# Performance work log

Hardware: AMD Instinct MI355X
Metric: run time of the kernel (lower is better)

## Reference

```python
import jax, jax.numpy as jnp
import numpy as np


def setup_inputs() -> dict:
    key = jax.random.key(0)
    k1, k2, k3, k4 = jax.random.split(key, 4)
    B, S, D = 4, 2048, 1024
    return {
        "x": jax.random.normal(k1, (B, S, D), dtype=jnp.float32),
        "wq": jax.random.normal(k2, (D, D), dtype=jnp.float32),
        "wk": jax.random.normal(k3, (D, D), dtype=jnp.float32),
        "wv": jax.random.normal(k4, (D, D), dtype=jnp.float32),
    }


def reference(x, wq, wk, wv):
    # q,k,v: [B,S,D]
    q = x @ wq
    k = x @ wk
    v = x @ wv
    # NOTE: source applies NO 1/sqrt(d) scaling; we match it faithfully.
    scores = jnp.einsum("bsd,btd->bst", q, k)  # [B,S,S]
    weights = jax.nn.softmax(scores, axis=-1)
    return jnp.einsum("bst,btd->bsd", weights, v)  # [B,S,D]
```

## Files before the change

kernel.cpp:

```cpp
#include <hip/hip_runtime.h>


typedef _Float16 half4_t __attribute__((ext_vector_type(4)));
typedef _Float16 half8_t __attribute__((ext_vector_type(8)));
typedef float f32x4 __attribute__((ext_vector_type(4)));

#define BM 128
#define BN 128
#define BK 32

__device__ __forceinline__ void gl_lds16(const _Float16* g, _Float16* l) {
    __builtin_amdgcn_global_load_lds(
        (const __attribute__((address_space(1))) unsigned int*)g,
        (__attribute__((address_space(3))) unsigned int*)l, 16, 0, 0);
}


__global__ __launch_bounds__(256) void conv_split_kernel(
    const float* __restrict__ in, _Float16* __restrict__ hi,
    _Float16* __restrict__ lo, int n4)
{
    int i = blockIdx.x * 256 + threadIdx.x;
    if (i >= n4) return;
    float4 v = ((const float4*)in)[i];
    float xs[4] = {v.x, v.y, v.z, v.w};
    half4_t h, l;
#pragma unroll
    for (int j = 0; j < 4; ++j) {
        _Float16 hh = (_Float16)xs[j];
        h[j] = hh;
        l[j] = (_Float16)(xs[j] - (float)hh);
    }
    ((half4_t*)hi)[i] = h;
    ((half4_t*)lo)[i] = l;
}

__global__ __launch_bounds__(256) void conv_wvT_kernel(
    const float* __restrict__ w, _Float16* __restrict__ oh)
{
    __shared__ float tle[64][65];
    const int tr = blockIdx.y * 64, tc = blockIdx.x * 64;
    const int t16 = threadIdx.x & 15, tq = threadIdx.x >> 4;
#pragma unroll
    for (int j = 0; j < 4; ++j) {
        int lr = tq + j * 16;
        float4 v = *(const float4*)(w + (size_t)(tr + lr) * 1024 + tc + t16 * 4);
        tle[lr][t16 * 4 + 0] = v.x;
        tle[lr][t16 * 4 + 1] = v.y;
        tle[lr][t16 * 4 + 2] = v.z;
        tle[lr][t16 * 4 + 3] = v.w;
    }
    __syncthreads();
#pragma unroll
    for (int j = 0; j < 4; ++j) {
        int orow = tq + j * 16;
        int oc = t16 * 4;
        half4_t h;
#pragma unroll
        for (int i = 0; i < 4; ++i) h[i] = (_Float16)tle[oc + i][orow];
        *(half4_t*)(oh + (size_t)(tc + orow) * 1024 + tr + oc) = h;
    }
}

template <bool OUTF32>
__global__ __launch_bounds__(256) void gemm_split(
    const _Float16* __restrict__ Ah, const _Float16* __restrict__ Al, size_t az,
    const _Float16* __restrict__ Bh, const _Float16* __restrict__ Bl, size_t bz,
    float* __restrict__ Cf, size_t cz, int ldc,
    _Float16* __restrict__ Oh, _Float16* __restrict__ Ol, size_t oz, int ldo,
    int lda, int ldb, int K)
{
    __shared__ __align__(16) _Float16 sAh[BM][BK], sAl[BM][BK];
    __shared__ __align__(16) _Float16 sBh[BN][BK], sBl[BN][BK];

    const int tid = threadIdx.x;
    const int wave = tid >> 6, lane = tid & 63;
    const int wm = (wave >> 1) * 64, wn = (wave & 1) * 64;
    const int lrow = lane & 15, quad = lane >> 4;
    const int bm = blockIdx.y * BM, bn = blockIdx.x * BN;
    const int z = blockIdx.z;

    const _Float16* pAh = Ah + (size_t)z * az;
    const _Float16* pAl = Al + (size_t)z * az;
    const _Float16* pBh = Bh + (size_t)z * bz;
    const _Float16* pBl = Bl + (size_t)z * bz;

    const int r0 = wave * 32 + (lane >> 2);
    const int kofs = (lane & 3) * 8;
    const size_t a0o = (size_t)(bm + r0) * lda + kofs;
    const size_t a1o = a0o + (size_t)16 * lda;
    const size_t b0o = (size_t)(bn + r0) * ldb + kofs;
    const size_t b1o = b0o + (size_t)16 * ldb;
    _Float16* lA0 = &sAh[r0][kofs];
    _Float16* lA1 = &sAh[r0 + 16][kofs];
    _Float16* lAl0 = &sAl[r0][kofs];
    _Float16* lAl1 = &sAl[r0 + 16][kofs];
    _Float16* lB0 = &sBh[r0][kofs];
    _Float16* lB1 = &sBh[r0 + 16][kofs];
    _Float16* lBl0 = &sBl[r0][kofs];
    _Float16* lBl1 = &sBl[r0 + 16][kofs];

    f32x4 acc[4][4];
#pragma unroll
    for (int i = 0; i < 4; ++i)
#pragma unroll
        for (int j = 0; j < 4; ++j) acc[i][j] = 0.0f;

    for (int k0 = 0; k0 < K; k0 += BK) {
        gl_lds16(pAh + a0o + k0, lA0);
        gl_lds16(pAh + a1o + k0, lA1);
        gl_lds16(pAl + a0o + k0, lAl0);
        gl_lds16(pAl + a1o + k0, lAl1);
        gl_lds16(pBh + b0o + k0, lB0);
        gl_lds16(pBh + b1o + k0, lB1);
        gl_lds16(pBl + b0o + k0, lBl0);
        gl_lds16(pBl + b1o + k0, lBl1);
        __syncthreads();

        half8_t a0[4], a1[4], b0[4], b1[4];
#pragma unroll
        for (int mt = 0; mt < 4; ++mt) {
            a0[mt] = *(const half8_t*)&sAh[wm + mt * 16 + lrow][quad * 8];
            a1[mt] = *(const half8_t*)&sAl[wm + mt * 16 + lrow][quad * 8];
        }
#pragma unroll
        for (int nt = 0; nt < 4; ++nt) {
            b0[nt] = *(const half8_t*)&sBh[wn + nt * 16 + lrow][quad * 8];
            b1[nt] = *(const half8_t*)&sBl[wn + nt * 16 + lrow][quad * 8];
        }
#pragma unroll
        for (int mt = 0; mt < 4; ++mt)
#pragma unroll
            for (int nt = 0; nt < 4; ++nt) {
                acc[mt][nt] = __builtin_amdgcn_mfma_f32_16x16x32_f16(a0[mt], b0[nt], acc[mt][nt], 0, 0, 0);
                acc[mt][nt] = __builtin_amdgcn_mfma_f32_16x16x32_f16(a0[mt], b1[nt], acc[mt][nt], 0, 0, 0);
                acc[mt][nt] = __builtin_amdgcn_mfma_f32_16x16x32_f16(a1[mt], b0[nt], acc[mt][nt], 0, 0, 0);
            }
        __syncthreads();
    }

#pragma unroll
    for (int mt = 0; mt < 4; ++mt)
#pragma unroll
        for (int nt = 0; nt < 4; ++nt)
#pragma unroll
            for (int r = 0; r < 4; ++r) {
                int gm = bm + wm + mt * 16 + quad * 4 + r;
                int gn = bn + wn + nt * 16 + lrow;
                float v = acc[mt][nt][r];
                if (OUTF32) {
                    Cf[(size_t)z * cz + (size_t)gm * ldc + gn] = v;
                } else {
                    _Float16 h = (_Float16)v;
                    Oh[(size_t)z * oz + (size_t)gm * ldo + gn] = h;
                    Ol[(size_t)z * oz + (size_t)gm * ldo + gn] = (_Float16)(v - (float)h);
                }
            }
}

template <bool TRANSOUT>
__global__ __launch_bounds__(256) void gemm_plain(
    const _Float16* __restrict__ Ag, size_t az,
    const _Float16* __restrict__ Bg, size_t bz,
    float* __restrict__ Cf, size_t cz, int ldc,
    _Float16* __restrict__ Ot,
    int lda, int ldb, int K)
{
    __shared__ __align__(16) _Float16 sA[BM][BK], sB[BN][BK];

    const int tid = threadIdx.x;
    const int wave = tid >> 6, lane = tid & 63;
    const int wm = (wave >> 1) * 64, wn = (wave & 1) * 64;
    const int lrow = lane & 15, quad = lane >> 4;
    const int bm = blockIdx.y * BM, bn = blockIdx.x * BN;
    const int z = blockIdx.z;

    const _Float16* pA = Ag + (size_t)z * az;
    const _Float16* pB = Bg + (size_t)z * bz;

    const int r0 = wave * 32 + (lane >> 2);
    const int kofs = (lane & 3) * 8;
    const size_t a0o = (size_t)(bm + r0) * lda + kofs;
    const size_t a1o = a0o + (size_t)16 * lda;
    const size_t b0o = (size_t)(bn + r0) * ldb + kofs;
    const size_t b1o = b0o + (size_t)16 * ldb;
    _Float16* lA0 = &sA[r0][kofs];
    _Float16* lA1 = &sA[r0 + 16][kofs];
    _Float16* lB0 = &sB[r0][kofs];
    _Float16* lB1 = &sB[r0 + 16][kofs];

    f32x4 acc[4][4];
#pragma unroll
    for (int i = 0; i < 4; ++i)
#pragma unroll
        for (int j = 0; j < 4; ++j) acc[i][j] = 0.0f;

    for (int k0 = 0; k0 < K; k0 += BK) {
        gl_lds16(pA + a0o + k0, lA0);
        gl_lds16(pA + a1o + k0, lA1);
        gl_lds16(pB + b0o + k0, lB0);
        gl_lds16(pB + b1o + k0, lB1);
        __syncthreads();

        half8_t a0[4], b0[4];
#pragma unroll
        for (int mt = 0; mt < 4; ++mt)
            a0[mt] = *(const half8_t*)&sA[wm + mt * 16 + lrow][quad * 8];
#pragma unroll
        for (int nt = 0; nt < 4; ++nt)
            b0[nt] = *(const half8_t*)&sB[wn + nt * 16 + lrow][quad * 8];
#pragma unroll
        for (int mt = 0; mt < 4; ++mt)
#pragma unroll
            for (int nt = 0; nt < 4; ++nt)
                acc[mt][nt] = __builtin_amdgcn_mfma_f32_16x16x32_f16(a0[mt], b0[nt], acc[mt][nt], 0, 0, 0);
        __syncthreads();
    }

#pragma unroll
    for (int mt = 0; mt < 4; ++mt)
#pragma unroll
        for (int nt = 0; nt < 4; ++nt) {
            int gm0 = bm + wm + mt * 16 + quad * 4;
            int gn = bn + wn + nt * 16 + lrow;
            if (TRANSOUT) {
                half4_t o;
#pragma unroll
                for (int r = 0; r < 4; ++r) o[r] = (_Float16)acc[mt][nt][r];
                *(half4_t*)(Ot + ((size_t)(gm0 >> 11) << 21) +
                            (size_t)gn * 2048 + (gm0 & 2047)) = o;
            } else {
#pragma unroll
                for (int r = 0; r < 4; ++r)
                    Cf[(size_t)z * cz + (size_t)(gm0 + r) * ldc + gn] = acc[mt][nt][r];
            }
        }
}

__global__ __launch_bounds__(256) void softmax_kernel(float* __restrict__ S)
{
    float* row = S + (size_t)blockIdx.x * 2048;
    float4* r4 = (float4*)row;
    const int tid = threadIdx.x;
    const int wave = tid >> 6, lane = tid & 63;

    float4 a = r4[tid], b = r4[tid + 256];
    float m = fmaxf(fmaxf(fmaxf(a.x, a.y), fmaxf(a.z, a.w)),
                    fmaxf(fmaxf(b.x, b.y), fmaxf(b.z, b.w)));
#pragma unroll
    for (int o = 32; o; o >>= 1) m = fmaxf(m, __shfl_xor(m, o));
    __shared__ float redm[4];
    __shared__ float reds[4];
    if (lane == 0) redm[wave] = m;
    __syncthreads();
    m = fmaxf(fmaxf(redm[0], redm[1]), fmaxf(redm[2], redm[3]));

    a.x = __expf(a.x - m); a.y = __expf(a.y - m);
    a.z = __expf(a.z - m); a.w = __expf(a.w - m);
    b.x = __expf(b.x - m); b.y = __expf(b.y - m);
    b.z = __expf(b.z - m); b.w = __expf(b.w - m);

    float s = a.x + a.y + a.z + a.w + b.x + b.y + b.z + b.w;
#pragma unroll
    for (int o = 32; o; o >>= 1) s += __shfl_xor(s, o);
    if (lane == 0) reds[wave] = s;
    __syncthreads();
    s = reds[0] + reds[1] + reds[2] + reds[3];

    float inv = 1.0f / s;
    _Float16* o16 = (_Float16*)row;
    half4_t ha, hb;
    ha[0] = (_Float16)(a.x * inv); ha[1] = (_Float16)(a.y * inv);
    ha[2] = (_Float16)(a.z * inv); ha[3] = (_Float16)(a.w * inv);
    hb[0] = (_Float16)(b.x * inv); hb[1] = (_Float16)(b.y * inv);
    hb[2] = (_Float16)(b.z * inv); hb[3] = (_Float16)(b.w * inv);
    ((half4_t*)o16)[tid] = ha;
    ((half4_t*)o16)[tid + 256] = hb;
}

extern "C" void kernel_launch(void* const* d_in, const int* in_sizes, int n_in,
                              void* d_out, int out_size, void* d_ws, size_t ws_size,
                              hipStream_t stream)
{
    const float* x  = (const float*)d_in[0];
    const float* wq = (const float*)d_in[1];
    const float* wk = (const float*)d_in[2];
    const float* wv = (const float*)d_in[3];
    float* out = (float*)d_out;

    const int S = 2048, D = 1024;
    const size_t M8 = 8ull << 20;
    const size_t M1 = 1ull << 20;
    char* ws = (char*)d_ws;

    _Float16* xh   = (_Float16*)(ws);
    _Float16* xl   = (_Float16*)(ws + (16ull << 20));
    _Float16* yh   = (_Float16*)(ws + (32ull << 20));
    _Float16* yl   = (_Float16*)(ws + (48ull << 20));
    _Float16* vT   = (_Float16*)(ws + (64ull << 20));
    _Float16* wqh  = (_Float16*)(ws + (80ull << 20));
    _Float16* wql  = (_Float16*)(ws + (82ull << 20));
    _Float16* wkh  = (_Float16*)(ws + (84ull << 20));
    _Float16* wkl  = (_Float16*)(ws + (86ull << 20));
    _Float16* wvTh = (_Float16*)(ws + (88ull << 20));
    _Float16* Mh   = (_Float16*)(ws + (90ull << 20));
    _Float16* Ml   = (_Float16*)(ws + (92ull << 20));
    float*    sc   = (float*)(ws + (94ull << 20));

    dim3 blk(256);

    conv_split_kernel<<<dim3((int)(M8 / 4 / 256)), blk, 0, stream>>>(x, xh, xl, (int)(M8 / 4));
    conv_split_kernel<<<dim3((int)(M1 / 4 / 256)), blk, 0, stream>>>(wq, wqh, wql, (int)(M1 / 4));
    conv_split_kernel<<<dim3((int)(M1 / 4 / 256)), blk, 0, stream>>>(wk, wkh, wkl, (int)(M1 / 4));
    conv_wvT_kernel<<<dim3(16, 16), blk, 0, stream>>>(wv, wvTh);

    gemm_split<false><<<dim3(8, 8, 1), blk, 0, stream>>>(
        wkh, wkl, 0, wqh, wql, 0, nullptr, 0, 0, Mh, Ml, 0, D, D, D, D);

    gemm_split<false><<<dim3(D / BN, 8192 / BM, 1), blk, 0, stream>>>(
        xh, xl, 0, Mh, Ml, 0, nullptr, 0, 0, yh, yl, 0, D, D, D, D);

    gemm_plain<true><<<dim3(D / BN, 8192 / BM, 1), blk, 0, stream>>>(
        xh, 0, wvTh, 0, nullptr, 0, 0, vT, D, D, D);

    gemm_split<true><<<dim3(S / BN, S / BM, 4), blk, 0, stream>>>(
        yh, yl, (size_t)S * D, xh, xl, (size_t)S * D, sc, (size_t)S * S, S,
        nullptr, nullptr, 0, 0, D, D, D);

    softmax_kernel<<<dim3(4 * S), blk, 0, stream>>>(sc);

    gemm_plain<false><<<dim3(D / BN, S / BM, 4), blk, 0, stream>>>(
        (const _Float16*)sc, (size_t)S * 4096, vT, (size_t)D * S,
        out, (size_t)S * D, D, nullptr, 4096, S, S);
}
```

Measured before the change: 431.9 us.

## Widen GEMM tiles to 128x256 with 8 waves and fuse conversion kernels

Doubles the GEMM block N-tile to 256 and runs 512 threads (8 waves in a 2x4 grid), with the global-to-LDS load mapping rewritten for the larger tile. Each wave still computes a 64x64 subtile, but every A tile loaded into LDS is now reused across twice as many columns. The four fp32-to-fp16 conversion and transpose launches are merged into one role-dispatched kernel to cut launch count. In exchange LDS per block doubles, fewer blocks fit on a CU, and the small weight GEMM launches fewer blocks.

```diff
diff --git a/kernel.cpp b/kernel.cpp
--- a/kernel.cpp
+++ b/kernel.cpp
@@ -6,7 +6,7 @@
 typedef float f32x4 __attribute__((ext_vector_type(4)));
 
 #define BM 128
-#define BN 128
+#define BN 256
 #define BK 32
 
 __device__ __forceinline__ void gl_lds16(const _Float16* g, _Float16* l) {
@@ -15,55 +15,62 @@
         (__attribute__((address_space(3))) unsigned int*)l, 16, 0, 0);
 }
 
-
-__global__ __launch_bounds__(256) void conv_split_kernel(
-    const float* __restrict__ in, _Float16* __restrict__ hi,
-    _Float16* __restrict__ lo, int n4)
-{
-    int i = blockIdx.x * 256 + threadIdx.x;
-    if (i >= n4) return;
-    float4 v = ((const float4*)in)[i];
-    float xs[4] = {v.x, v.y, v.z, v.w};
-    half4_t h, l;
-#pragma unroll
-    for (int j = 0; j < 4; ++j) {
-        _Float16 hh = (_Float16)xs[j];
-        h[j] = hh;
-        l[j] = (_Float16)(xs[j] - (float)hh);
+__global__ __launch_bounds__(256) void conv_all_kernel(
+    const float* __restrict__ x, const float* __restrict__ wq,
+    const float* __restrict__ wk, const float* __restrict__ wv,
+    _Float16* __restrict__ xh, _Float16* __restrict__ xl,
+    _Float16* __restrict__ qh, _Float16* __restrict__ ql,
+    _Float16* __restrict__ kh, _Float16* __restrict__ kl,
+    _Float16* __restrict__ vTh)
+{
+    __shared__ float tle[64][65];
+    const int role = blockIdx.y;
+    if (role < 3) {
+        const float* in = (role == 0) ? x : (role == 1) ? wq : wk;
+        _Float16* hi = (role == 0) ? xh : (role == 1) ? qh : kh;
+        _Float16* lo = (role == 0) ? xl : (role == 1) ? ql : kl;
+        const int n4 = (role == 0) ? (1 << 21) : (1 << 18);
+        int i = blockIdx.x * 256 + threadIdx.x;
+        if (i >= n4) return;
+        float4 v = ((const float4*)in)[i];
+        float xs[4] = {v.x, v.y, v.z, v.w};
+        half4_t h, l;
+#pragma unroll
+        for (int j = 0; j < 4; ++j) {
+            _Float16 hh = (_Float16)xs[j];
+            h[j] = hh;
+            l[j] = (_Float16)(xs[j] - (float)hh);
+        }
+        ((half4_t*)hi)[i] = h;
+        ((half4_t*)lo)[i] = l;
+    } else {
+        if (blockIdx.x >= 256) return;
+        const int tr = (blockIdx.x >> 4) * 64, tc = (blockIdx.x & 15) * 64;
+        const int t16 = threadIdx.x & 15, tq = threadIdx.x >> 4;
+#pragma unroll
+        for (int j = 0; j < 4; ++j) {
+            int lr = tq + j * 16;
+            float4 v = *(const float4*)(wv + (size_t)(tr + lr) * 1024 + tc + t16 * 4);
+            tle[lr][t16 * 4 + 0] = v.x;
+            tle[lr][t16 * 4 + 1] = v.y;
+            tle[lr][t16 * 4 + 2] = v.z;
+            tle[lr][t16 * 4 + 3] = v.w;
+        }
+        __syncthreads();
+#pragma unroll
+        for (int j = 0; j < 4; ++j) {
+            int orow = tq + j * 16;
+            int oc = t16 * 4;
+            half4_t h;
+#pragma unroll
+            for (int i = 0; i < 4; ++i) h[i] = (_Float16)tle[oc + i][orow];
+            *(half4_t*)(vTh + (size_t)(tc + orow) * 1024 + tr + oc) = h;
+        }
     }
-    ((half4_t*)hi)[i] = h;
-    ((half4_t*)lo)[i] = l;
-}
-
-__global__ __launch_bounds__(256) void conv_wvT_kernel(
-    const float* __restrict__ w, _Float16* __restrict__ oh)
-{
-    __shared__ float tle[64][65];
-    const int tr = blockIdx.y * 64, tc = blockIdx.x * 64;
-    const int t16 = threadIdx.x & 15, tq = threadIdx.x >> 4;
-#pragma unroll
-    for (int j = 0; j < 4; ++j) {
-        int lr = tq + j * 16;
-        float4 v = *(const float4*)(w + (size_t)(tr + lr) * 1024 + tc + t16 * 4);
-        tle[lr][t16 * 4 + 0] = v.x;
-        tle[lr][t16 * 4 + 1] = v.y;
-        tle[lr][t16 * 4 + 2] = v.z;
-        tle[lr][t16 * 4 + 3] = v.w;
-    }
-    __syncthreads();
-#pragma unroll
-    for (int j = 0; j < 4; ++j) {
-        int orow = tq + j * 16;
-        int oc = t16 * 4;
-        half4_t h;
-#pragma unroll
-        for (int i = 0; i < 4; ++i) h[i] = (_Float16)tle[oc + i][orow];
-        *(half4_t*)(oh + (size_t)(tc + orow) * 1024 + tr + oc) = h;
-    }
 }
 
 template <bool OUTF32>
-__global__ __launch_bounds__(256) void gemm_split(
+__global__ __launch_bounds__(512, 5) void gemm_split(
     const _Float16* __restrict__ Ah, const _Float16* __restrict__ Al, size_t az,
     const _Float16* __restrict__ Bh, const _Float16* __restrict__ Bl, size_t bz,
     float* __restrict__ Cf, size_t cz, int ldc,
@@ -75,7 +82,7 @@
 
     const int tid = threadIdx.x;
     const int wave = tid >> 6, lane = tid & 63;
-    const int wm = (wave >> 1) * 64, wn = (wave & 1) * 64;
+    const int wm = (wave >> 2) * 64, wn = (wave & 3) * 64;
     const int lrow = lane & 15, quad = lane >> 4;
     const int bm = blockIdx.y * BM, bn = blockIdx.x * BN;
     const int z = blockIdx.z;
@@ -85,20 +92,17 @@
     const _Float16* pBh = Bh + (size_t)z * bz;
     const _Float16* pBl = Bl + (size_t)z * bz;
 
-    const int r0 = wave * 32 + (lane >> 2);
-    const int kofs = (lane & 3) * 8;
-    const size_t a0o = (size_t)(bm + r0) * lda + kofs;
-    const size_t a1o = a0o + (size_t)16 * lda;
-    const size_t b0o = (size_t)(bn + r0) * ldb + kofs;
-    const size_t b1o = b0o + (size_t)16 * ldb;
-    _Float16* lA0 = &sAh[r0][kofs];
-    _Float16* lA1 = &sAh[r0 + 16][kofs];
-    _Float16* lAl0 = &sAl[r0][kofs];
-    _Float16* lAl1 = &sAl[r0 + 16][kofs];
-    _Float16* lB0 = &sBh[r0][kofs];
-    _Float16* lB1 = &sBh[r0 + 16][kofs];
-    _Float16* lBl0 = &sBl[r0][kofs];
-    _Float16* lBl1 = &sBl[r0 + 16][kofs];
+    const int rowA = tid >> 2;
+    const int kofs = (tid & 3) * 8;
+    const size_t aoff  = (size_t)(bm + rowA) * lda + kofs;
+    const size_t boff0 = (size_t)(bn + rowA) * ldb + kofs;
+    const size_t boff1 = boff0 + (size_t)128 * ldb;
+    _Float16* lAh = &sAh[rowA][kofs];
+    _Float16* lAl = &sAl[rowA][kofs];
+    _Float16* lBh0 = &sBh[rowA][kofs];
+    _Float16* lBh1 = &sBh[rowA + 128][kofs];
+    _Float16* lBl0 = &sBl[rowA][kofs];
+    _Float16* lBl1 = &sBl[rowA + 128][kofs];
 
     f32x4 acc[4][4];
 #pragma unroll
@@ -107,14 +111,12 @@
         for (int j = 0; j < 4; ++j) acc[i][j] = 0.0f;
 
     for (int k0 = 0; k0 < K; k0 += BK) {
-        gl_lds16(pAh + a0o + k0, lA0);
-        gl_lds16(pAh + a1o + k0, lA1);
-        gl_lds16(pAl + a0o + k0, lAl0);
-        gl_lds16(pAl + a1o + k0, lAl1);
-        gl_lds16(pBh + b0o + k0, lB0);
-        gl_lds16(pBh + b1o + k0, lB1);
-        gl_lds16(pBl + b0o + k0, lBl0);
-        gl_lds16(pBl + b1o + k0, lBl1);
+        gl_lds16(pAh + aoff + k0, lAh);
+        gl_lds16(pAl + aoff + k0, lAl);
+        gl_lds16(pBh + boff0 + k0, lBh0);
+        gl_lds16(pBh + boff1 + k0, lBh1);
+        gl_lds16(pBl + boff0 + k0, lBl0);
+        gl_lds16(pBl + boff1 + k0, lBl1);
         __syncthreads();
 
         half8_t a0[4], a1[4], b0[4], b1[4];
@@ -159,7 +161,7 @@
 }
 
 template <bool TRANSOUT>
-__global__ __launch_bounds__(256) void gemm_plain(
+__global__ __launch_bounds__(512, 5) void gemm_plain(
     const _Float16* __restrict__ Ag, size_t az,
     const _Float16* __restrict__ Bg, size_t bz,
     float* __restrict__ Cf, size_t cz, int ldc,
@@ -170,7 +172,7 @@
 
     const int tid = threadIdx.x;
     const int wave = tid >> 6, lane = tid & 63;
-    const int wm = (wave >> 1) * 64, wn = (wave & 1) * 64;
+    const int wm = (wave >> 2) * 64, wn = (wave & 3) * 64;
     const int lrow = lane & 15, quad = lane >> 4;
     const int bm = blockIdx.y * BM, bn = blockIdx.x * BN;
     const int z = blockIdx.z;
@@ -178,16 +180,14 @@
     const _Float16* pA = Ag + (size_t)z * az;
     const _Float16* pB = Bg + (size_t)z * bz;
 
-    const int r0 = wave * 32 + (lane >> 2);
-    const int kofs = (lane & 3) * 8;
-    const size_t a0o = (size_t)(bm + r0) * lda + kofs;
-    const size_t a1o = a0o + (size_t)16 * lda;
-    const size_t b0o = (size_t)(bn + r0) * ldb + kofs;
-    const size_t b1o = b0o + (size_t)16 * ldb;
-    _Float16* lA0 = &sA[r0][kofs];
-    _Float16* lA1 = &sA[r0 + 16][kofs];
-    _Float16* lB0 = &sB[r0][kofs];
-    _Float16* lB1 = &sB[r0 + 16][kofs];
+    const int rowA = tid >> 2;
+    const int kofs = (tid & 3) * 8;
+    const size_t aoff  = (size_t)(bm + rowA) * lda + kofs;
+    const size_t boff0 = (size_t)(bn + rowA) * ldb + kofs;
+    const size_t boff1 = boff0 + (size_t)128 * ldb;
+    _Float16* lA  = &sA[rowA][kofs];
+    _Float16* lB0 = &sB[rowA][kofs];
+    _Float16* lB1 = &sB[rowA + 128][kofs];
 
     f32x4 acc[4][4];
 #pragma unroll
@@ -196,10 +196,9 @@
         for (int j = 0; j < 4; ++j) acc[i][j] = 0.0f;
 
     for (int k0 = 0; k0 < K; k0 += BK) {
-        gl_lds16(pA + a0o + k0, lA0);
-        gl_lds16(pA + a1o + k0, lA1);
-        gl_lds16(pB + b0o + k0, lB0);
-        gl_lds16(pB + b1o + k0, lB1);
+        gl_lds16(pA + aoff + k0, lA);
+        gl_lds16(pB + boff0 + k0, lB0);
+        gl_lds16(pB + boff1 + k0, lB1);
         __syncthreads();
 
         half8_t a0[4], b0[4];
@@ -289,8 +288,6 @@
     float* out = (float*)d_out;
 
     const int S = 2048, D = 1024;
-    const size_t M8 = 8ull << 20;
-    const size_t M1 = 1ull << 20;
     char* ws = (char*)d_ws;
 
     _Float16* xh   = (_Float16*)(ws);
@@ -307,29 +304,25 @@
     _Float16* Ml   = (_Float16*)(ws + (92ull << 20));
     float*    sc   = (float*)(ws + (94ull << 20));
 
-    dim3 blk(256);
-
-    conv_split_kernel<<<dim3((int)(M8 / 4 / 256)), blk, 0, stream>>>(x, xh, xl, (int)(M8 / 4));
-    conv_split_kernel<<<dim3((int)(M1 / 4 / 256)), blk, 0, stream>>>(wq, wqh, wql, (int)(M1 / 4));
-    conv_split_kernel<<<dim3((int)(M1 / 4 / 256)), blk, 0, stream>>>(wk, wkh, wkl, (int)(M1 / 4));
-    conv_wvT_kernel<<<dim3(16, 16), blk, 0, stream>>>(wv, wvTh);
-
-    gemm_split<false><<<dim3(8, 8, 1), blk, 0, stream>>>(
+    conv_all_kernel<<<dim3(8192, 4), dim3(256), 0, stream>>>(
+        x, wq, wk, wv, xh, xl, wqh, wql, wkh, wkl, wvTh);
+
+    gemm_split<false><<<dim3(D / BN, D / BM, 1), dim3(512), 0, stream>>>(
         wkh, wkl, 0, wqh, wql, 0, nullptr, 0, 0, Mh, Ml, 0, D, D, D, D);
 
-    gemm_split<false><<<dim3(D / BN, 8192 / BM, 1), blk, 0, stream>>>(
+    gemm_split<false><<<dim3(D / BN, 8192 / BM, 1), dim3(512), 0, stream>>>(
         xh, xl, 0, Mh, Ml, 0, nullptr, 0, 0, yh, yl, 0, D, D, D, D);
 
-    gemm_plain<true><<<dim3(D / BN, 8192 / BM, 1), blk, 0, stream>>>(
+    gemm_plain<true><<<dim3(D / BN, 8192 / BM, 1), dim3(512), 0, stream>>>(
         xh, 0, wvTh, 0, nullptr, 0, 0, vT, D, D, D);
 
-    gemm_split<true><<<dim3(S / BN, S / BM, 4), blk, 0, stream>>>(
+    gemm_split<true><<<dim3(S / BN, S / BM, 4), dim3(512), 0, stream>>>(
         yh, yl, (size_t)S * D, xh, xl, (size_t)S * D, sc, (size_t)S * S, S,
         nullptr, nullptr, 0, 0, D, D, D);
 
-    softmax_kernel<<<dim3(4 * S), blk, 0, stream>>>(sc);
-
-    gemm_plain<false><<<dim3(D / BN, S / BM, 4), blk, 0, stream>>>(
+    softmax_kernel<<<dim3(4 * S), dim3(256), 0, stream>>>(sc);
+
+    gemm_plain<false><<<dim3(D / BN, S / BM, 4), dim3(512), 0, stream>>>(
         (const _Float16*)sc, (size_t)S * 4096, vT, (size_t)D * S,
         out, (size_t)S * D, D, nullptr, 4096, S, S);
 }
```

Result: slower. 991.3 us (+129.5%).

## Load low-part GEMM fragments straight from global memory and fuse conversion kernels

Applied to the files above, without the earlier changes.

The split-precision GEMM no longer stages the low halves of A and B in LDS. Each wave loads its lo fragments directly from global memory into registers, and only the hi halves go through LDS, which halves shared-memory footprint and LDS traffic. This may allow higher occupancy. The four input-conversion kernels are merged into one launch, where blockIdx.y selects the role. The trade-off is uncoalesced 16-byte global reads of the lo fragments, which are loaded redundantly across waves.

```diff
diff --git a/kernel.cpp b/kernel.cpp
--- a/kernel.cpp
+++ b/kernel.cpp
@@ -15,50 +15,57 @@
         (__attribute__((address_space(3))) unsigned int*)l, 16, 0, 0);
 }
 
-
-__global__ __launch_bounds__(256) void conv_split_kernel(
-    const float* __restrict__ in, _Float16* __restrict__ hi,
-    _Float16* __restrict__ lo, int n4)
-{
-    int i = blockIdx.x * 256 + threadIdx.x;
-    if (i >= n4) return;
-    float4 v = ((const float4*)in)[i];
-    float xs[4] = {v.x, v.y, v.z, v.w};
-    half4_t h, l;
-#pragma unroll
-    for (int j = 0; j < 4; ++j) {
-        _Float16 hh = (_Float16)xs[j];
-        h[j] = hh;
-        l[j] = (_Float16)(xs[j] - (float)hh);
-    }
-    ((half4_t*)hi)[i] = h;
-    ((half4_t*)lo)[i] = l;
-}
-
-__global__ __launch_bounds__(256) void conv_wvT_kernel(
-    const float* __restrict__ w, _Float16* __restrict__ oh)
+__global__ __launch_bounds__(256) void conv_all_kernel(
+    const float* __restrict__ x, const float* __restrict__ wq,
+    const float* __restrict__ wk, const float* __restrict__ wv,
+    _Float16* __restrict__ xh, _Float16* __restrict__ xl,
+    _Float16* __restrict__ qh, _Float16* __restrict__ ql,
+    _Float16* __restrict__ kh, _Float16* __restrict__ kl,
+    _Float16* __restrict__ vTh)
 {
     __shared__ float tle[64][65];
-    const int tr = blockIdx.y * 64, tc = blockIdx.x * 64;
-    const int t16 = threadIdx.x & 15, tq = threadIdx.x >> 4;
-#pragma unroll
-    for (int j = 0; j < 4; ++j) {
-        int lr = tq + j * 16;
-        float4 v = *(const float4*)(w + (size_t)(tr + lr) * 1024 + tc + t16 * 4);
-        tle[lr][t16 * 4 + 0] = v.x;
-        tle[lr][t16 * 4 + 1] = v.y;
-        tle[lr][t16 * 4 + 2] = v.z;
-        tle[lr][t16 * 4 + 3] = v.w;
-    }
-    __syncthreads();
-#pragma unroll
-    for (int j = 0; j < 4; ++j) {
-        int orow = tq + j * 16;
-        int oc = t16 * 4;
-        half4_t h;
-#pragma unroll
-        for (int i = 0; i < 4; ++i) h[i] = (_Float16)tle[oc + i][orow];
-        *(half4_t*)(oh + (size_t)(tc + orow) * 1024 + tr + oc) = h;
+    const int role = blockIdx.y;
+    if (role < 3) {
+        const float* in = (role == 0) ? x : (role == 1) ? wq : wk;
+        _Float16* hi = (role == 0) ? xh : (role == 1) ? qh : kh;
+        _Float16* lo = (role == 0) ? xl : (role == 1) ? ql : kl;
+        const int n4 = (role == 0) ? (1 << 21) : (1 << 18);
+        int i = blockIdx.x * 256 + threadIdx.x;
+        if (i >= n4) return;
+        float4 v = ((const float4*)in)[i];
+        float xs[4] = {v.x, v.y, v.z, v.w};
+        half4_t h, l;
+#pragma unroll
+        for (int j = 0; j < 4; ++j) {
+            _Float16 hh = (_Float16)xs[j];
+            h[j] = hh;
+            l[j] = (_Float16)(xs[j] - (float)hh);
+        }
+        ((half4_t*)hi)[i] = h;
+        ((half4_t*)lo)[i] = l;
+    } else {
+        if (blockIdx.x >= 256) return;
+        const int tr = (blockIdx.x >> 4) * 64, tc = (blockIdx.x & 15) * 64;
+        const int t16 = threadIdx.x & 15, tq = threadIdx.x >> 4;
+#pragma unroll
+        for (int j = 0; j < 4; ++j) {
+            int lr = tq + j * 16;
+            float4 v = *(const float4*)(wv + (size_t)(tr + lr) * 1024 + tc + t16 * 4);
+            tle[lr][t16 * 4 + 0] = v.x;
+            tle[lr][t16 * 4 + 1] = v.y;
+            tle[lr][t16 * 4 + 2] = v.z;
+            tle[lr][t16 * 4 + 3] = v.w;
+        }
+        __syncthreads();
+#pragma unroll
+        for (int j = 0; j < 4; ++j) {
+            int orow = tq + j * 16;
+            int oc = t16 * 4;
+            half4_t h;
+#pragma unroll
+            for (int i = 0; i < 4; ++i) h[i] = (_Float16)tle[oc + i][orow];
+            *(half4_t*)(vTh + (size_t)(tc + orow) * 1024 + tr + oc) = h;
+        }
     }
 }
 
@@ -70,8 +77,8 @@
     _Float16* __restrict__ Oh, _Float16* __restrict__ Ol, size_t oz, int ldo,
     int lda, int ldb, int K)
 {
-    __shared__ __align__(16) _Float16 sAh[BM][BK], sAl[BM][BK];
-    __shared__ __align__(16) _Float16 sBh[BN][BK], sBl[BN][BK];
+    __shared__ __align__(16) _Float16 sAh[BM][BK];
+    __shared__ __align__(16) _Float16 sBh[BN][BK];
 
     const int tid = threadIdx.x;
     const int wave = tid >> 6, lane = tid & 63;
@@ -93,12 +100,11 @@
     const size_t b1o = b0o + (size_t)16 * ldb;
     _Float16* lA0 = &sAh[r0][kofs];
     _Float16* lA1 = &sAh[r0 + 16][kofs];
-    _Float16* lAl0 = &sAl[r0][kofs];
-    _Float16* lAl1 = &sAl[r0 + 16][kofs];
     _Float16* lB0 = &sBh[r0][kofs];
     _Float16* lB1 = &sBh[r0 + 16][kofs];
-    _Float16* lBl0 = &sBl[r0][kofs];
-    _Float16* lBl1 = &sBl[r0 + 16][kofs];
+
+    const size_t alo = (size_t)(bm + wm + lrow) * lda + quad * 8;
+    const size_t blo = (size_t)(bn + wn + lrow) * ldb + quad * 8;
 
     f32x4 acc[4][4];
 #pragma unroll
@@ -109,33 +115,42 @@
     for (int k0 = 0; k0 < K; k0 += BK) {
         gl_lds16(pAh + a0o + k0, lA0);
         gl_lds16(pAh + a1o + k0, lA1);
-        gl_lds16(pAl + a0o + k0, lAl0);
-        gl_lds16(pAl + a1o + k0, lAl1);
         gl_lds16(pBh + b0o + k0, lB0);
         gl_lds16(pBh + b1o + k0, lB1);
-        gl_lds16(pBl + b0o + k0, lBl0);
-        gl_lds16(pBl + b1o + k0, lBl1);
-        __syncthreads();
-
-        half8_t a0[4], a1[4], b0[4], b1[4];
-#pragma unroll
-        for (int mt = 0; mt < 4; ++mt) {
-            a0[mt] = *(const half8_t*)&sAh[wm + mt * 16 + lrow][quad * 8];
-            a1[mt] = *(const half8_t*)&sAl[wm + mt * 16 + lrow][quad * 8];
-        }
-#pragma unroll
-        for (int nt = 0; nt < 4; ++nt) {
-            b0[nt] = *(const half8_t*)&sBh[wn + nt * 16 + lrow][quad * 8];
-            b1[nt] = *(const half8_t*)&sBl[wn + nt * 16 + lrow][quad * 8];
-        }
-#pragma unroll
-        for (int mt = 0; mt < 4; ++mt)
-#pragma unroll
-            for (int nt = 0; nt < 4; ++nt) {
-                acc[mt][nt] = __builtin_amdgcn_mfma_f32_16x16x32_f16(a0[mt], b0[nt], acc[mt][nt], 0, 0, 0);
-                acc[mt][nt] = __builtin_amdgcn_mfma_f32_16x16x32_f16(a0[mt], b1[nt], acc[mt][nt], 0, 0, 0);
-                acc[mt][nt] = __builtin_amdgcn_mfma_f32_16x16x32_f16(a1[mt], b0[nt], acc[mt][nt], 0, 0, 0);
-            }
+
+        half8_t aL[4], bL[4];
+#pragma unroll
+        for (int mt = 0; mt < 4; ++mt)
+            aL[mt] = *(const half8_t*)(pAl + alo + (size_t)mt * 16 * lda + k0);
+#pragma unroll
+        for (int nt = 0; nt < 4; ++nt)
+            bL[nt] = *(const half8_t*)(pBl + blo + (size_t)nt * 16 * ldb + k0);
+
+        __syncthreads();
+
+        half8_t aH[4], bH[4];
+#pragma unroll
+        for (int mt = 0; mt < 4; ++mt)
+            aH[mt] = *(const half8_t*)&sAh[wm + mt * 16 + lrow][quad * 8];
+#pragma unroll
+        for (int nt = 0; nt < 4; ++nt)
+            bH[nt] = *(const half8_t*)&sBh[wn + nt * 16 + lrow][quad * 8];
+
+#pragma unroll
+        for (int mt = 0; mt < 4; ++mt)
+#pragma unroll
+            for (int nt = 0; nt < 4; ++nt)
+                acc[mt][nt] = __builtin_amdgcn_mfma_f32_16x16x32_f16(aH[mt], bH[nt], acc[mt][nt], 0, 0, 0);
+#pragma unroll
+        for (int mt = 0; mt < 4; ++mt)
+#pragma unroll
+            for (int nt = 0; nt < 4; ++nt)
+                acc[mt][nt] = __builtin_amdgcn_mfma_f32_16x16x32_f16(aH[mt], bL[nt], acc[mt][nt], 0, 0, 0);
+#pragma unroll
+        for (int mt = 0; mt < 4; ++mt)
+#pragma unroll
+            for (int nt = 0; nt < 4; ++nt)
+                acc[mt][nt] = __builtin_amdgcn_mfma_f32_16x16x32_f16(aL[mt], bH[nt], acc[mt][nt], 0, 0, 0);
         __syncthreads();
     }
 
@@ -289,8 +304,6 @@
     float* out = (float*)d_out;
 
     const int S = 2048, D = 1024;
-    const size_t M8 = 8ull << 20;
-    const size_t M1 = 1ull << 20;
     char* ws = (char*)d_ws;
 
     _Float16* xh   = (_Float16*)(ws);
@@ -307,29 +320,25 @@
     _Float16* Ml   = (_Float16*)(ws + (92ull << 20));
     float*    sc   = (float*)(ws + (94ull << 20));
 
-    dim3 blk(256);
-
-    conv_split_kernel<<<dim3((int)(M8 / 4 / 256)), blk, 0, stream>>>(x, xh, xl, (int)(M8 / 4));
-    conv_split_kernel<<<dim3((int)(M1 / 4 / 256)), blk, 0, stream>>>(wq, wqh, wql, (int)(M1 / 4));
-    conv_split_kernel<<<dim3((int)(M1 / 4 / 256)), blk, 0, stream>>>(wk, wkh, wkl, (int)(M1 / 4));
-    conv_wvT_kernel<<<dim3(16, 16), blk, 0, stream>>>(wv, wvTh);
-
-    gemm_split<false><<<dim3(8, 8, 1), blk, 0, stream>>>(
+    conv_all_kernel<<<dim3(8192, 4), dim3(256), 0, stream>>>(
+        x, wq, wk, wv, xh, xl, wqh, wql, wkh, wkl, wvTh);
+
+    gemm_split<false><<<dim3(D / BN, D / BM, 1), dim3(256), 0, stream>>>(
         wkh, wkl, 0, wqh, wql, 0, nullptr, 0, 0, Mh, Ml, 0, D, D, D, D);
 
-    gemm_split<false><<<dim3(D / BN, 8192 / BM, 1), blk, 0, stream>>>(
+    gemm_split<false><<<dim3(D / BN, 8192 / BM, 1), dim3(256), 0, stream>>>(
         xh, xl, 0, Mh, Ml, 0, nullptr, 0, 0, yh, yl, 0, D, D, D, D);
 
-    gemm_plain<true><<<dim3(D / BN, 8192 / BM, 1), blk, 0, stream>>>(
+    gemm_plain<true><<<dim3(D / BN, 8192 / BM, 1), dim3(256), 0, stream>>>(
         xh, 0, wvTh, 0, nullptr, 0, 0, vT, D, D, D);
 
-    gemm_split<true><<<dim3(S / BN, S / BM, 4), blk, 0, stream>>>(
+    gemm_split<true><<<dim3(S / BN, S / BM, 4), dim3(256), 0, stream>>>(
         yh, yl, (size_t)S * D, xh, xl, (size_t)S * D, sc, (size_t)S * S, S,
         nullptr, nullptr, 0, 0, D, D, D);
 
-    softmax_kernel<<<dim3(4 * S), blk, 0, stream>>>(sc);
-
-    gemm_plain<false><<<dim3(D / BN, S / BM, 4), blk, 0, stream>>>(
+    softmax_kernel<<<dim3(4 * S), dim3(256), 0, stream>>>(sc);
+
+    gemm_plain<false><<<dim3(D / BN, S / BM, 4), dim3(256), 0, stream>>>(
         (const _Float16*)sc, (size_t)S * 4096, vT, (size_t)D * S,
         out, (size_t)S * D, D, nullptr, 4096, S, S);
 }
```

Measured after the change: 493.0 us. 14.2% more time.
